# Performance work log

Hardware: AMD Instinct MI355X
Metric: run time of the kernel (lower is better)

## Reference

```python
import jax, jax.numpy as jnp
import numpy as np
from jax import lax

B, T, E, H, V = 1024, 128, 300, 100, 50000
K = 4  # topk in catch()
NEG_INF = -1e30


def setup_inputs() -> dict:
    key = jax.random.key(0)
    ks = jax.random.split(key, 12)
    word_id = jax.random.randint(ks[0], (B, T), 0, V, dtype=jnp.int32)
    sen_len = jax.random.randint(ks[1], (B,), K, T + 1, dtype=jnp.int32)  # >= K for topk
    label_word_id = jax.random.randint(ks[2], (B, 1), 0, V, dtype=jnp.int32)
    emb = jax.random.normal(ks[3], (V, E), jnp.float32) * 0.1
    W_ih = jax.random.normal(ks[4], (4 * H, E), jnp.float32) * 0.05
    W_hh = jax.random.normal(ks[5], (4 * H, H), jnp.float32) * 0.05
    b_ih = jax.random.normal(ks[6], (4 * H,), jnp.float32) * 0.05
    b_hh = jax.random.normal(ks[7], (4 * H,), jnp.float32) * 0.05
    lin_W = jax.random.normal(ks[8], (6, H), jnp.float32) * 0.1
    lin_b = jax.random.normal(ks[9], (6,), jnp.float32) * 0.1
    ll_W = jax.random.normal(ks[10], (H, E), jnp.float32) * 0.05
    ll_b = jax.random.normal(ks[11], (H,), jnp.float32) * 0.05
    return dict(word_id=word_id, sen_len=sen_len, label_word_id=label_word_id,
                emb=emb, W_ih=W_ih, W_hh=W_hh, b_ih=b_ih, b_hh=b_hh,
                lin_W=lin_W, lin_b=lin_b, ll_W=ll_W, ll_b=ll_b)


def _lstm(x, W_ih, W_hh, b_ih, b_hh):
    # x: (B, T, E) -> out: (B, T, H). Single layer, pytorch gate order i,f,g,o.
    b = b_ih + b_hh
    def step(carry, x_t):
        h, c = carry
        gates = x_t @ W_ih.T + h @ W_hh.T + b  # (B, 4H)
        i, f, g, o = jnp.split(gates, 4, axis=-1)
        c = jax.nn.sigmoid(f) * c + jax.nn.sigmoid(i) * jnp.tanh(g)
        h = jax.nn.sigmoid(o) * jnp.tanh(c)
        return (h, c), h
    h0 = jnp.zeros((x.shape[0], W_hh.shape[1]), x.dtype)
    (_, _), hs = lax.scan(step, (h0, h0), x.transpose(1, 0, 2))
    return hs.transpose(1, 0, 2)


def reference(word_id, sen_len, label_word_id, emb, W_ih, W_hh, b_ih, b_hh,
              lin_W, lin_b, ll_W, ll_b):
    word_vec = emb[word_id]                      # (B, T, E)
    out = _lstm(word_vec, W_ih, W_hh, b_ih, b_hh)  # (B, T, H)

    # last valid hidden state -> linear
    last = out[jnp.arange(out.shape[0]), sen_len - 1]  # (B, H)
    out_f = last @ lin_W.T + lin_b               # (B, 6)

    # label vector through llinear
    label_vec = emb[label_word_id[:, 0]] @ ll_W.T + ll_b  # (B, H)

    # --- catch(), vectorized ---
    scores = jnp.einsum('bth,bh->bt', out, label_vec)     # (B, T)
    valid = jnp.arange(out.shape[1])[None, :] < sen_len[:, None]  # (B, T)
    vals, idx = lax.top_k(jnp.where(valid, scores, NEG_INF), K)   # (B, K)
    s_value = jnp.take_along_axis(out, idx[:, :, None], axis=1)   # (B, K, H)
    pos = jnp.sum(s_value * vals[:, :, None], axis=1)             # (B, H)

    # neg: valid positions excluding topk; original bug: vector_list accumulates
    # across the batch loop -> cumulative sum over batch dimension.
    top_mask = jnp.zeros(valid.shape, bool).at[
        jnp.arange(valid.shape[0])[:, None], idx].set(True)
    neg_mask = valid & ~top_mask                                   # (B, T)
    per_neg = jnp.einsum('bth,bt->bh', out, neg_mask.astype(out.dtype))
    neg = jnp.cumsum(per_neg, axis=0)                              # (B, H)

    l_rep = pos @ lin_W.T + lin_b
    r_rep = neg @ lin_W.T + lin_b
    return (out_f, l_rep, r_rep)
```

## Files before the change

### kernel.cpp

```cpp
#include <hip/hip_runtime.h>
#include <hip/hip_bf16.h>
#include <cstdint>

#define Bn   1024
#define Tn   128
#define En   300
#define Hn   100
#define Vn   50000
#define G4n  400
#define MPn  50048
#define NPn  448

typedef __bf16 bf16x8 __attribute__((ext_vector_type(8)));
typedef _Float16 half8 __attribute__((ext_vector_type(8)));
typedef _Float16 half2v __attribute__((ext_vector_type(2)));
typedef float  f32x4  __attribute__((ext_vector_type(4)));

#define OFF_TABLE  0ull
#define OFF_OH16   44800000ull
#define OFF_WFRAG  71014400ull
#define OFF_WFRAGB 71129088ull
#define OFF_LLWT   71415808ull
#define OFF_LV     71535808ull
#define OFF_PN     71945408ull
#define OFF_NEG    72355008ull

__device__ __forceinline__ float sigf(float x) { return 1.0f / (1.0f + __expf(-x)); }
__device__ __forceinline__ float tanhfast(float x) { return 1.0f - 2.0f / (__expf(2.0f * x) + 1.0f); }

__global__ void k_prep(const float* __restrict__ W_ih, const float* __restrict__ W_hh,
                       const float* __restrict__ llW,
                       uint4* __restrict__ wfrag, uint4* __restrict__ wfragB,
                       float* __restrict__ llwt) {
    int idx = blockIdx.x * 256 + threadIdx.x;
    if (idx < 28 * 4 * 64) {
        int lane = idx & 63, tk = idx >> 6;
        int nt = tk >> 2, kc = tk & 3;
        int n = nt * 16 + (lane & 15);
        int k0 = kc * 32 + (lane >> 4) * 8;
        int q = n & 3, u = n >> 2;
        union { _Float16 h[8]; uint4 v; } pk;
#pragma unroll
        for (int j = 0; j < 8; j++) {
            int k = k0 + j;
            pk.h[j] = (_Float16)((u < Hn && k < Hn) ? W_hh[(size_t)(q * Hn + u) * Hn + k] : 0.0f);
        }
        wfrag[idx] = pk.v;
    }
    if (idx < 10 * 28 * 64) {
        int lane = idx & 63, tk = idx >> 6;
        int kc = tk / 28, nsg = tk - kc * 28;
        int n = nsg * 16 + (lane & 15);
        int k0 = kc * 32 + (lane >> 4) * 8;
        int q = n & 3, u = n >> 2;
        union { __bf16 h[8]; uint4 v; } pk;
#pragma unroll
        for (int j = 0; j < 8; j++) {
            int k = k0 + j;
            pk.h[j] = (__bf16)((u < Hn && k < En) ? W_ih[(size_t)(q * Hn + u) * En + k] : 0.0f);
        }
        wfragB[idx] = pk.v;
    }
    if (idx < En * Hn) {
        int k = idx / Hn, h = idx - k * Hn;
        llwt[idx] = llW[(size_t)h * En + k];
    }
}

__global__ __launch_bounds__(256, 2) void k_table(
    const float* __restrict__ emb, const uint4* __restrict__ wfragB,
    const float* __restrict__ b_ih, const float* __restrict__ b_hh,
    _Float16* __restrict__ table) {
    __shared__ __bf16 a_sh[64][328];
    const int tid = threadIdx.x;
    const int mt = blockIdx.x >> 1, nh = blockIdx.x & 1;

#pragma unroll
    for (int it = 0; it < 5; it++) {
        int x = it * 256 + tid;
        int row = x / 20, seg = x - row * 20;
        int gr = mt * 64 + row;
        const float* ar = emb + (size_t)(gr < Vn ? gr : Vn - 1) * En;
        int c0 = seg * 16;
        union { __bf16 h[16]; bf16x8 v[2]; } pk;
#pragma unroll
        for (int g = 0; g < 4; g++) {
            int c = c0 + g * 4;
            if (c + 4 <= En) {
                float4 f = *(const float4*)(ar + c);
                pk.h[g * 4 + 0] = (__bf16)f.x; pk.h[g * 4 + 1] = (__bf16)f.y;
                pk.h[g * 4 + 2] = (__bf16)f.z; pk.h[g * 4 + 3] = (__bf16)f.w;
            } else {
                pk.h[g * 4 + 0] = (__bf16)0.f; pk.h[g * 4 + 1] = (__bf16)0.f;
                pk.h[g * 4 + 2] = (__bf16)0.f; pk.h[g * 4 + 3] = (__bf16)0.f;
            }
        }
        *(bf16x8*)&a_sh[row][c0] = pk.v[0];
        *(bf16x8*)&a_sh[row][c0 + 8] = pk.v[1];
    }
    __syncthreads();

    const int wv = tid >> 6, l = tid & 63;
    const int c16 = l & 15, quad = l >> 4;
    f32x4 acc[14];
#pragma unroll
    for (int i = 0; i < 14; i++) acc[i] = (f32x4){0.f, 0.f, 0.f, 0.f};

    uint4 bcur[14];
#pragma unroll
    for (int ns = 0; ns < 14; ns++) bcur[ns] = wfragB[((0 * 28 + nh * 14 + ns) << 6) + l];

    for (int kc = 0; kc < 10; kc++) {
        uint4 bnxt[14];
        if (kc < 9) {
#pragma unroll
            for (int ns = 0; ns < 14; ns++) bnxt[ns] = wfragB[(((kc + 1) * 28 + nh * 14 + ns) << 6) + l];
        }
        bf16x8 af = *(const bf16x8*)&a_sh[wv * 16 + c16][kc * 32 + quad * 8];
#pragma unroll
        for (int ns = 0; ns < 14; ns++)
            acc[ns] = __builtin_amdgcn_mfma_f32_16x16x32_bf16(af, __builtin_bit_cast(bf16x8, bcur[ns]), acc[ns], 0, 0, 0);
        if (kc < 9) {
#pragma unroll
            for (int ns = 0; ns < 14; ns++) bcur[ns] = bnxt[ns];
        }
    }
#pragma unroll
    for (int ns = 0; ns < 14; ns++) {
        int n = (nh * 14 + ns) * 16 + c16;
        int q = n & 3, u = n >> 2;
        if (u < Hn) {
            int j = q * Hn + u;
            float bias = b_ih[j] + b_hh[j];
#pragma unroll
            for (int r = 0; r < 4; r++) {
                int m = mt * 64 + wv * 16 + quad * 4 + r;
                if (m < Vn) table[(size_t)m * NPn + n] = (_Float16)(acc[ns][r] + bias);
            }
        }
    }
}

__global__ void k_label(const int* __restrict__ lwid, const float* __restrict__ emb,
                        const float* __restrict__ llwt, const float* __restrict__ llb,
                        float* __restrict__ lv) {
    __shared__ float er[En];
    __shared__ float part[Hn];
    int b = blockIdx.x;
    int lid = lwid[b];
    for (int k = threadIdx.x; k < En; k += 256) er[k] = emb[(size_t)lid * En + k];
    __syncthreads();
    int h = threadIdx.x & 127, half = threadIdx.x >> 7;
    float acc = 0.f;
    if (h < Hn) {
        int k0 = half * 150, k1 = k0 + 150;
        for (int k = k0; k < k1; k++) acc += er[k] * llwt[k * Hn + h];
        if (half == 1) part[h] = acc;
    }
    __syncthreads();
    if (h < Hn && half == 0) lv[(size_t)b * Hn + h] = acc + part[h] + llb[h];
}

__global__ __launch_bounds__(256, 2) void k_lstm(
    const int* __restrict__ word_id, const int* __restrict__ sen_len,
    const _Float16* __restrict__ table, const uint4* __restrict__ wfrag,
    const float* __restrict__ lv, const float* __restrict__ linW,
    const float* __restrict__ linb, _Float16* __restrict__ oh16,
    float* __restrict__ per_neg, float* __restrict__ d_out) {
    __shared__ float    gbufs[4][280];
    __shared__ _Float16 h_cur[2][2][136];
    __shared__ float    lt_sh[2][Hn];
    __shared__ float    spw[2][Tn][4];
    __shared__ int      widc[2][Tn];
    __shared__ float    pos_sh[2][Hn];
    __shared__ float    lasth_sh[2][Hn];
    __shared__ float    tk_val[2][4];
    __shared__ int      tk_idx[2][4];

    const int tid = threadIdx.x;
    const int w = tid >> 6, l = tid & 63;
    const int c16 = l & 15, quad = l >> 4;
    const int b0 = blockIdx.x * 2;

    for (int i = tid; i < 272; i += 256) ((uint32_t*)h_cur)[i] = 0u;
    if (tid < 200) {
        int imb = (tid >= Hn), iu = tid - imb * Hn;
        lt_sh[imb][iu] = lv[(size_t)(b0 + imb) * Hn + iu];
    }
    { int imb = tid >> 7, it = tid & 127; widc[imb][it] = word_id[(b0 + imb) * Tn + it]; }

    half8 bfr[7][4];
#pragma unroll
    for (int n7 = 0; n7 < 7; n7++)
#pragma unroll
        for (int kc = 0; kc < 4; kc++)
            bfr[n7][kc] = __builtin_bit_cast(half8, wfrag[((w * 7 + n7) * 4 + kc) * 64 + l]);

    const int u_loc = l >> 1, mb = l & 1;
    const int u = w * 28 + u_loc;
    const bool act = (l < 56) && (u < Hn);
    const int myslen = act ? sen_len[b0 + mb] : 0;
    float* gb = &gbufs[w][0];

    __syncthreads();

    uint2 xq = {0, 0};
    if (act) xq = *(const uint2*)(table + (size_t)widc[mb][0] * NPn + u * 4);

    float c_reg = 0.f, sumh = 0.f, lasth = 0.f;
    _Float16* ohb_w = oh16 + (size_t)(b0 + mb) * Tn * Hn;

    for (int t = 0; t < Tn; t++) {
        const _Float16* hp = &h_cur[t & 1][0][0];
        f32x4 acc[7];
#pragma unroll
        for (int n7 = 0; n7 < 7; n7++) acc[n7] = (f32x4){0.f, 0.f, 0.f, 0.f};
#pragma unroll
        for (int kc = 0; kc < 4; kc++) {
            half8 af = *(const half8*)(hp + (c16 & 1) * 136 + kc * 32 + quad * 8);
#pragma unroll
            for (int n7 = 0; n7 < 7; n7++)
                acc[n7] = __builtin_amdgcn_mfma_f32_16x16x32_f16(af, bfr[n7][kc], acc[n7], 0, 0, 0);
        }
        if (l < 16) {
#pragma unroll
            for (int n7 = 0; n7 < 7; n7++) {
                int nl = n7 * 16 + l;
                int adr = (nl >> 2) * 5 + (nl & 3);
                gb[adr] = acc[n7][0];
                gb[140 + adr] = acc[n7][1];
            }
        }
        float p = 0.f;
        if (act) {
            int base = mb * 140 + u_loc * 5;
            half2v x01 = __builtin_bit_cast(half2v, xq.x);
            half2v x23 = __builtin_bit_cast(half2v, xq.y);
            float gi = gb[base] + (float)x01.x;
            float gf = gb[base + 1] + (float)x01.y;
            float gg = gb[base + 2] + (float)x23.x;
            float go = gb[base + 3] + (float)x23.y;
            float c = sigf(gf) * c_reg + sigf(gi) * tanhfast(gg);
            c_reg = c;
            float hh = sigf(go) * tanhfast(c);
            h_cur[(t + 1) & 1][mb][u] = (_Float16)hh;
            ohb_w[t * Hn + u] = (_Float16)hh;
            if (t < myslen) sumh += hh;
            if (t == myslen - 1) lasth = hh;
            p = hh * lt_sh[mb][u];
            int tn = (t + 1 < Tn) ? t + 1 : t;
            xq = *(const uint2*)(table + (size_t)widc[mb][tn] * NPn + u * 4);
        }
        p += __shfl_down(p, 32, 64);
        p += __shfl_down(p, 16, 64);
        p += __shfl_down(p, 8, 64);
        p += __shfl_down(p, 4, 64);
        p += __shfl_down(p, 2, 64);
        if (l < 2) spw[l][t][w] = p;
        __syncthreads();
    }
    if (w < 2) {
        int kmb = w, lane = l;
        int sl = sen_len[b0 + kmb];
        float4 p0 = *(const float4*)&spw[kmb][lane][0];
        float4 p1 = *(const float4*)&spw[kmb][lane + 64][0];
        float s0 = (lane < sl) ? (p0.x + p0.y + p0.z + p0.w) : -1e30f;
        float s1 = (lane + 64 < sl) ? (p1.x + p1.y + p1.z + p1.w) : -1e30f;
        bool tk0 = false, tk1 = false;
#pragma unroll
        for (int p4 = 0; p4 < 4; p4++) {
            float v = tk0 ? -1e30f : s0;
            int ix = lane;
            float v1 = tk1 ? -1e30f : s1;
            if (v1 > v) { v = v1; ix = lane + 64; }
            for (int off = 32; off; off >>= 1) {
                float ov = __shfl_down(v, off, 64);
                int oi = __shfl_down(ix, off, 64);
                if (ov > v || (ov == v && oi < ix)) { v = ov; ix = oi; }
            }
            v = __shfl(v, 0, 64);
            ix = __shfl(ix, 0, 64);
            if (lane == 0) { tk_val[kmb][p4] = v; tk_idx[kmb][p4] = ix; }
            if (ix == lane) tk0 = true;
            if (ix == lane + 64) tk1 = true;
        }
    }
    __syncthreads();
    if (act) {
        float pos = 0.f, nsum = sumh;
#pragma unroll
        for (int p4 = 0; p4 < 4; p4++) {
            int ix = tk_idx[mb][p4];
            float r = (float)ohb_w[ix * Hn + u];
            pos += tk_val[mb][p4] * r;
            nsum -= r;
        }
        pos_sh[mb][u] = pos;
        lasth_sh[mb][u] = lasth;
        per_neg[(size_t)(b0 + mb) * Hn + u] = nsum;
    }
    __syncthreads();
    if (tid < 24) {
        int which = tid / 12, r = tid - which * 12;
        int pmb = r / 6, o = r - pmb * 6;
        const float* src = which ? &pos_sh[pmb][0] : &lasth_sh[pmb][0];
        float acc2 = linb[o];
        for (int uu = 0; uu < Hn; uu++) acc2 += src[uu] * linW[o * Hn + uu];
        d_out[(which ? (Bn * 6) : 0) + (b0 + pmb) * 6 + o] = acc2;
    }
}

__global__ __launch_bounds__(1024) void k_scan(const float* __restrict__ pn, float* __restrict__ neg) {
    __shared__ float wsum[16];
    __shared__ float wpre[16];
    int u = blockIdx.x, t = threadIdx.x;
    int lane = t & 63, wv = t >> 6;
    float v = pn[(size_t)t * Hn + u];
#pragma unroll
    for (int off = 1; off < 64; off <<= 1) {
        float o = __shfl_up(v, off, 64);
        if (lane >= off) v += o;
    }
    if (lane == 63) wsum[wv] = v;
    __syncthreads();
    if (t < 16) {
        float s = wsum[t];
#pragma unroll
        for (int off = 1; off < 16; off <<= 1) {
            float o = __shfl_up(s, off, 64);
            if (t >= off) s += o;
        }
        wpre[t] = s;
    }
    __syncthreads();
    float pre = wv ? wpre[wv - 1] : 0.f;
    neg[(size_t)t * Hn + u] = v + pre;
}

__global__ void k_rrep(const float* __restrict__ neg, const float* __restrict__ linW,
                       const float* __restrict__ linb, float* __restrict__ d_out) {
    int gid = blockIdx.x * 256 + threadIdx.x;
    if (gid < Bn * 6) {
        int b = gid / 6, o = gid - b * 6;
        float acc = linb[o];
        for (int u = 0; u < Hn; u++) acc += neg[(size_t)b * Hn + u] * linW[o * Hn + u];
        d_out[2 * Bn * 6 + gid] = acc;
    }
}

extern "C" void kernel_launch(void* const* d_in, const int* in_sizes, int n_in,
                              void* d_out, int out_size, void* d_ws, size_t ws_size,
                              hipStream_t stream) {
    const int*   word_id = (const int*)d_in[0];
    const int*   sen_len = (const int*)d_in[1];
    const int*   lwid    = (const int*)d_in[2];
    const float* emb     = (const float*)d_in[3];
    const float* W_ih    = (const float*)d_in[4];
    const float* W_hh    = (const float*)d_in[5];
    const float* b_ih    = (const float*)d_in[6];
    const float* b_hh    = (const float*)d_in[7];
    const float* linW    = (const float*)d_in[8];
    const float* linb    = (const float*)d_in[9];
    const float* llW     = (const float*)d_in[10];
    const float* llb     = (const float*)d_in[11];

    char* ws = (char*)d_ws;
    _Float16* table  = (_Float16*)(ws + OFF_TABLE);
    _Float16* oh16   = (_Float16*)(ws + OFF_OH16);
    uint4*    wfrag  = (uint4*)(ws + OFF_WFRAG);
    uint4*    wfragB = (uint4*)(ws + OFF_WFRAGB);
    float*    llwt   = (float*)(ws + OFF_LLWT);
    float*    lvp    = (float*)(ws + OFF_LV);
    float*    pn     = (float*)(ws + OFF_PN);
    float*    neg    = (float*)(ws + OFF_NEG);
    float*    outp   = (float*)d_out;

    k_prep<<<118, 256, 0, stream>>>(W_ih, W_hh, llW, wfrag, wfragB, llwt);
    k_table<<<(MPn / 64) * 2, 256, 0, stream>>>(emb, wfragB, b_ih, b_hh, table);
    k_label<<<Bn, 256, 0, stream>>>(lwid, emb, llwt, llb, lvp);
    k_lstm<<<Bn / 2, 256, 0, stream>>>(word_id, sen_len, table, wfrag, lvp, linW, linb, oh16, pn, outp);
    k_scan<<<Hn, 1024, 0, stream>>>(pn, neg);
    k_rrep<<<(Bn * 6 + 255) / 256, 256, 0, stream>>>(neg, linW, linb, outp);
}
```

Baseline: 309.3 us.

## Batch four sequences per LSTM block and move label projection to MFMA

The LSTM kernel now processes four sequences per 512-thread block. Seven waves compute all gate columns with MFMA for the four rows, and an eighth wave computes the label-attention scores for the previous step in parallel, where before each wave reduced scores inline. The label linear projection is rewritten as a bf16 MFMA GEMM over 64-row tiles using prepacked weight fragments, replacing one block per sample. This makes better use of the 16-row MFMA tiles and halves the number of LSTM blocks. In exchange it adds two barriers per timestep and uses bf16 precision for the label vector.

```diff
diff --git a/kernel.cpp b/kernel.cpp
--- a/kernel.cpp
+++ b/kernel.cpp
@@ -20,7 +20,7 @@
 #define OFF_OH16   44800000ull
 #define OFF_WFRAG  71014400ull
 #define OFF_WFRAGB 71129088ull
-#define OFF_LLWT   71415808ull
+#define OFF_WFRL   71415808ull
 #define OFF_LV     71535808ull
 #define OFF_PN     71945408ull
 #define OFF_NEG    72355008ull
@@ -31,7 +31,7 @@
 __global__ void k_prep(const float* __restrict__ W_ih, const float* __restrict__ W_hh,
                        const float* __restrict__ llW,
                        uint4* __restrict__ wfrag, uint4* __restrict__ wfragB,
-                       float* __restrict__ llwt) {
+                       uint4* __restrict__ wfragL) {
     int idx = blockIdx.x * 256 + threadIdx.x;
     if (idx < 28 * 4 * 64) {
         int lane = idx & 63, tk = idx >> 6;
@@ -61,9 +61,18 @@
         }
         wfragB[idx] = pk.v;
     }
-    if (idx < En * Hn) {
-        int k = idx / Hn, h = idx - k * Hn;
-        llwt[idx] = llW[(size_t)h * En + k];
+    if (idx < 10 * 7 * 64) {
+        int lane = idx & 63, tk = idx >> 6;
+        int kc = tk / 7, nsg = tk - kc * 7;
+        int n = nsg * 16 + (lane & 15);
+        int k0 = kc * 32 + (lane >> 4) * 8;
+        union { __bf16 h[8]; uint4 v; } pk;
+#pragma unroll
+        for (int j = 0; j < 8; j++) {
+            int k = k0 + j;
+            pk.h[j] = (__bf16)((n < Hn && k < En) ? llW[(size_t)n * En + k] : 0.0f);
+        }
+        wfragL[idx] = pk.v;
     }
 }
 
@@ -141,67 +150,106 @@
     }
 }
 
-__global__ void k_label(const int* __restrict__ lwid, const float* __restrict__ emb,
-                        const float* __restrict__ llwt, const float* __restrict__ llb,
-                        float* __restrict__ lv) {
-    __shared__ float er[En];
-    __shared__ float part[Hn];
-    int b = blockIdx.x;
-    int lid = lwid[b];
-    for (int k = threadIdx.x; k < En; k += 256) er[k] = emb[(size_t)lid * En + k];
-    __syncthreads();
-    int h = threadIdx.x & 127, half = threadIdx.x >> 7;
-    float acc = 0.f;
-    if (h < Hn) {
-        int k0 = half * 150, k1 = k0 + 150;
-        for (int k = k0; k < k1; k++) acc += er[k] * llwt[k * Hn + h];
-        if (half == 1) part[h] = acc;
-    }
-    __syncthreads();
-    if (h < Hn && half == 0) lv[(size_t)b * Hn + h] = acc + part[h] + llb[h];
-}
-
-__global__ __launch_bounds__(256, 2) void k_lstm(
+__global__ __launch_bounds__(256, 2) void k_label(
+    const int* __restrict__ lwid, const float* __restrict__ emb,
+    const uint4* __restrict__ wfragL, const float* __restrict__ llb,
+    float* __restrict__ lv) {
+    __shared__ __bf16 a_sh[64][328];
+    const int tid = threadIdx.x;
+    const int b0 = blockIdx.x * 64;
+
+#pragma unroll
+    for (int it = 0; it < 5; it++) {
+        int x = it * 256 + tid;
+        int row = x / 20, seg = x - row * 20;
+        int lid = lwid[b0 + row];
+        const float* ar = emb + (size_t)lid * En;
+        int c0 = seg * 16;
+        union { __bf16 h[16]; bf16x8 v[2]; } pk;
+#pragma unroll
+        for (int g = 0; g < 4; g++) {
+            int c = c0 + g * 4;
+            if (c + 4 <= En) {
+                float4 f = *(const float4*)(ar + c);
+                pk.h[g * 4 + 0] = (__bf16)f.x; pk.h[g * 4 + 1] = (__bf16)f.y;
+                pk.h[g * 4 + 2] = (__bf16)f.z; pk.h[g * 4 + 3] = (__bf16)f.w;
+            } else {
+                pk.h[g * 4 + 0] = (__bf16)0.f; pk.h[g * 4 + 1] = (__bf16)0.f;
+                pk.h[g * 4 + 2] = (__bf16)0.f; pk.h[g * 4 + 3] = (__bf16)0.f;
+            }
+        }
+        *(bf16x8*)&a_sh[row][c0] = pk.v[0];
+        *(bf16x8*)&a_sh[row][c0 + 8] = pk.v[1];
+    }
+    __syncthreads();
+
+    const int wv = tid >> 6, l = tid & 63;
+    const int c16 = l & 15, quad = l >> 4;
+    f32x4 acc[7];
+#pragma unroll
+    for (int i = 0; i < 7; i++) acc[i] = (f32x4){0.f, 0.f, 0.f, 0.f};
+    for (int kc = 0; kc < 10; kc++) {
+        bf16x8 af = *(const bf16x8*)&a_sh[wv * 16 + c16][kc * 32 + quad * 8];
+#pragma unroll
+        for (int ns = 0; ns < 7; ns++) {
+            bf16x8 bf = __builtin_bit_cast(bf16x8, wfragL[((kc * 7 + ns) << 6) + l]);
+            acc[ns] = __builtin_amdgcn_mfma_f32_16x16x32_bf16(af, bf, acc[ns], 0, 0, 0);
+        }
+    }
+#pragma unroll
+    for (int ns = 0; ns < 7; ns++) {
+        int n = ns * 16 + c16;
+        if (n < Hn) {
+            float bias = llb[n];
+#pragma unroll
+            for (int r = 0; r < 4; r++) {
+                int m = b0 + wv * 16 + quad * 4 + r;
+                lv[(size_t)m * Hn + n] = acc[ns][r] + bias;
+            }
+        }
+    }
+}
+
+__global__ __launch_bounds__(512, 2) void k_lstm(
     const int* __restrict__ word_id, const int* __restrict__ sen_len,
     const _Float16* __restrict__ table, const uint4* __restrict__ wfrag,
     const float* __restrict__ lv, const float* __restrict__ linW,
     const float* __restrict__ linb, _Float16* __restrict__ oh16,
     float* __restrict__ per_neg, float* __restrict__ d_out) {
-    __shared__ float    gbufs[4][280];
-    __shared__ _Float16 h_cur[2][2][136];
-    __shared__ float    lt_sh[2][Hn];
-    __shared__ float    spw[2][Tn][4];
-    __shared__ int      widc[2][Tn];
-    __shared__ float    pos_sh[2][Hn];
-    __shared__ float    lasth_sh[2][Hn];
-    __shared__ float    tk_val[2][4];
-    __shared__ int      tk_idx[2][4];
+    __shared__ float    g_sh[4 * 452];
+    __shared__ _Float16 h_cur[2][16][136];
+    __shared__ float    lt_sh[4][Hn];
+    __shared__ float    scores_sh[4][Tn];
+    __shared__ int      widc[4][Tn];
+    __shared__ float    pos_sh[4][Hn];
+    __shared__ float    lasth_sh[4][Hn];
+    __shared__ float    tk_val[4][4];
+    __shared__ int      tk_idx[4][4];
 
     const int tid = threadIdx.x;
     const int w = tid >> 6, l = tid & 63;
     const int c16 = l & 15, quad = l >> 4;
-    const int b0 = blockIdx.x * 2;
-
-    for (int i = tid; i < 272; i += 256) ((uint32_t*)h_cur)[i] = 0u;
-    if (tid < 200) {
-        int imb = (tid >= Hn), iu = tid - imb * Hn;
+    const int b0 = blockIdx.x * 4;
+
+    for (int i = tid; i < 2 * 16 * 136 / 2; i += 512) ((uint32_t*)h_cur)[i] = 0u;
+    if (tid < 400) {
+        int imb = tid / 100, iu = tid - imb * 100;
         lt_sh[imb][iu] = lv[(size_t)(b0 + imb) * Hn + iu];
     }
     { int imb = tid >> 7, it = tid & 127; widc[imb][it] = word_id[(b0 + imb) * Tn + it]; }
 
-    half8 bfr[7][4];
-#pragma unroll
-    for (int n7 = 0; n7 < 7; n7++)
-#pragma unroll
-        for (int kc = 0; kc < 4; kc++)
-            bfr[n7][kc] = __builtin_bit_cast(half8, wfrag[((w * 7 + n7) * 4 + kc) * 64 + l]);
-
-    const int u_loc = l >> 1, mb = l & 1;
-    const int u = w * 28 + u_loc;
-    const bool act = (l < 56) && (u < Hn);
+    half8 bfr[4][4];
+    if (w < 7) {
+#pragma unroll
+        for (int j = 0; j < 4; j++)
+#pragma unroll
+            for (int kc = 0; kc < 4; kc++)
+                bfr[j][kc] = __builtin_bit_cast(half8, wfrag[((w * 4 + j) * 4 + kc) * 64 + l]);
+    }
+
+    const int mb = tid & 3, u = tid >> 2;
+    const bool act = (tid < 400);
     const int myslen = act ? sen_len[b0 + mb] : 0;
-    float* gb = &gbufs[w][0];
-
     __syncthreads();
 
     uint2 xq = {0, 0};
@@ -211,61 +259,82 @@
     _Float16* ohb_w = oh16 + (size_t)(b0 + mb) * Tn * Hn;
 
     for (int t = 0; t < Tn; t++) {
-        const _Float16* hp = &h_cur[t & 1][0][0];
-        f32x4 acc[7];
-#pragma unroll
-        for (int n7 = 0; n7 < 7; n7++) acc[n7] = (f32x4){0.f, 0.f, 0.f, 0.f};
-#pragma unroll
-        for (int kc = 0; kc < 4; kc++) {
-            half8 af = *(const half8*)(hp + (c16 & 1) * 136 + kc * 32 + quad * 8);
-#pragma unroll
-            for (int n7 = 0; n7 < 7; n7++)
-                acc[n7] = __builtin_amdgcn_mfma_f32_16x16x32_f16(af, bfr[n7][kc], acc[n7], 0, 0, 0);
-        }
-        if (l < 16) {
-#pragma unroll
-            for (int n7 = 0; n7 < 7; n7++) {
-                int nl = n7 * 16 + l;
-                int adr = (nl >> 2) * 5 + (nl & 3);
-                gb[adr] = acc[n7][0];
-                gb[140 + adr] = acc[n7][1];
-            }
-        }
-        float p = 0.f;
+        const int pin = t & 1;
+        if (w < 7) {
+            const _Float16* hp = &h_cur[pin][0][0];
+            f32x4 acc[4];
+#pragma unroll
+            for (int j = 0; j < 4; j++) acc[j] = (f32x4){0.f, 0.f, 0.f, 0.f};
+#pragma unroll
+            for (int kc = 0; kc < 4; kc++) {
+                half8 af = *(const half8*)(hp + c16 * 136 + kc * 32 + quad * 8);
+#pragma unroll
+                for (int j = 0; j < 4; j++)
+                    acc[j] = __builtin_amdgcn_mfma_f32_16x16x32_f16(af, bfr[j][kc], acc[j], 0, 0, 0);
+            }
+            if (l < 16) {
+#pragma unroll
+                for (int j = 0; j < 4; j++) {
+                    int n = (w * 4 + j) * 16 + l;
+#pragma unroll
+                    for (int r = 0; r < 4; r++) g_sh[r * 452 + n] = acc[j][r];
+                }
+            }
+        } else if (t > 0) {
+            int smb = l & 3, u0 = l >> 2;
+            float p = 0.f;
+#pragma unroll
+            for (int i = 0; i < 7; i++) {
+                int uu = u0 + 16 * i;
+                if (uu < Hn) p += (float)h_cur[pin][smb][uu] * lt_sh[smb][uu];
+            }
+            p += __shfl_down(p, 32, 64);
+            p += __shfl_down(p, 16, 64);
+            p += __shfl_down(p, 8, 64);
+            p += __shfl_down(p, 4, 64);
+            if (l < 4) scores_sh[smb][t - 1] = p;
+        }
+        __syncthreads();
         if (act) {
-            int base = mb * 140 + u_loc * 5;
+            float4 g4 = *(const float4*)&g_sh[mb * 452 + u * 4];
             half2v x01 = __builtin_bit_cast(half2v, xq.x);
             half2v x23 = __builtin_bit_cast(half2v, xq.y);
-            float gi = gb[base] + (float)x01.x;
-            float gf = gb[base + 1] + (float)x01.y;
-            float gg = gb[base + 2] + (float)x23.x;
-            float go = gb[base + 3] + (float)x23.y;
+            float gi = g4.x + (float)x01.x;
+            float gf = g4.y + (float)x01.y;
+            float gg = g4.z + (float)x23.x;
+            float go = g4.w + (float)x23.y;
             float c = sigf(gf) * c_reg + sigf(gi) * tanhfast(gg);
             c_reg = c;
             float hh = sigf(go) * tanhfast(c);
-            h_cur[(t + 1) & 1][mb][u] = (_Float16)hh;
+            h_cur[pin ^ 1][mb][u] = (_Float16)hh;
             ohb_w[t * Hn + u] = (_Float16)hh;
             if (t < myslen) sumh += hh;
             if (t == myslen - 1) lasth = hh;
-            p = hh * lt_sh[mb][u];
             int tn = (t + 1 < Tn) ? t + 1 : t;
             xq = *(const uint2*)(table + (size_t)widc[mb][tn] * NPn + u * 4);
+        }
+        __syncthreads();
+    }
+    if (w == 7) {
+        int smb = l & 3, u0 = l >> 2;
+        float p = 0.f;
+#pragma unroll
+        for (int i = 0; i < 7; i++) {
+            int uu = u0 + 16 * i;
+            if (uu < Hn) p += (float)h_cur[0][smb][uu] * lt_sh[smb][uu];
         }
         p += __shfl_down(p, 32, 64);
         p += __shfl_down(p, 16, 64);
         p += __shfl_down(p, 8, 64);
         p += __shfl_down(p, 4, 64);
-        p += __shfl_down(p, 2, 64);
-        if (l < 2) spw[l][t][w] = p;
-        __syncthreads();
-    }
-    if (w < 2) {
+        if (l < 4) scores_sh[smb][Tn - 1] = p;
+    }
+    __syncthreads();
+    if (w < 4) {
         int kmb = w, lane = l;
         int sl = sen_len[b0 + kmb];
-        float4 p0 = *(const float4*)&spw[kmb][lane][0];
-        float4 p1 = *(const float4*)&spw[kmb][lane + 64][0];
-        float s0 = (lane < sl) ? (p0.x + p0.y + p0.z + p0.w) : -1e30f;
-        float s1 = (lane + 64 < sl) ? (p1.x + p1.y + p1.z + p1.w) : -1e30f;
+        float s0 = (lane < sl) ? scores_sh[kmb][lane] : -1e30f;
+        float s1 = (lane + 64 < sl) ? scores_sh[kmb][lane + 64] : -1e30f;
         bool tk0 = false, tk1 = false;
 #pragma unroll
         for (int p4 = 0; p4 < 4; p4++) {
@@ -300,8 +369,8 @@
         per_neg[(size_t)(b0 + mb) * Hn + u] = nsum;
     }
     __syncthreads();
-    if (tid < 24) {
-        int which = tid / 12, r = tid - which * 12;
+    if (tid < 48) {
+        int which = tid / 24, r = tid - which * 24;
         int pmb = r / 6, o = r - pmb * 6;
         const float* src = which ? &pos_sh[pmb][0] : &lasth_sh[pmb][0];
         float acc2 = linb[o];
@@ -369,16 +438,16 @@
     _Float16* oh16   = (_Float16*)(ws + OFF_OH16);
     uint4*    wfrag  = (uint4*)(ws + OFF_WFRAG);
     uint4*    wfragB = (uint4*)(ws + OFF_WFRAGB);
-    float*    llwt   = (float*)(ws + OFF_LLWT);
+    uint4*    wfragL = (uint4*)(ws + OFF_WFRL);
     float*    lvp    = (float*)(ws + OFF_LV);
     float*    pn     = (float*)(ws + OFF_PN);
     float*    neg    = (float*)(ws + OFF_NEG);
     float*    outp   = (float*)d_out;
 
-    k_prep<<<118, 256, 0, stream>>>(W_ih, W_hh, llW, wfrag, wfragB, llwt);
+    k_prep<<<70, 256, 0, stream>>>(W_ih, W_hh, llW, wfrag, wfragB, wfragL);
     k_table<<<(MPn / 64) * 2, 256, 0, stream>>>(emb, wfragB, b_ih, b_hh, table);
-    k_label<<<Bn, 256, 0, stream>>>(lwid, emb, llwt, llb, lvp);
-    k_lstm<<<Bn / 2, 256, 0, stream>>>(word_id, sen_len, table, wfrag, lvp, linW, linb, oh16, pn, outp);
+    k_label<<<Bn / 64, 256, 0, stream>>>(lwid, emb, wfragL, llb, lvp);
+    k_lstm<<<Bn / 4, 512, 0, stream>>>(word_id, sen_len, table, wfrag, lvp, linW, linb, oh16, pn, outp);
     k_scan<<<Hn, 1024, 0, stream>>>(pn, neg);
     k_rrep<<<(Bn * 6 + 255) / 256, 256, 0, stream>>>(neg, linW, linb, outp);
 }
```

Measured after the change: 315.8 us. +2.1%, slower.
